# Performance work log

Hardware: AMD Instinct MI355X
Metric: run time of the kernel (lower is better)

## Reference

```python
import jax, jax.numpy as jnp
import numpy as np

ALPHA = 1.0
TOL = 1e-5
MAX_ITER = 50
M = 0.05  # monotonicity margin of MONSingleFc


def setup_inputs() -> dict:
    key = jax.random.key(0)
    kx, ku, kub, ka, kb = jax.random.split(key, 5)
    batch, in_dim, d = 65536, 128, 128
    x = jax.random.normal(kx, (batch, in_dim), jnp.float32)
    Uw = jax.random.normal(ku, (d, in_dim), jnp.float32) / np.sqrt(in_dim)
    ub = jax.random.normal(kub, (d,), jnp.float32) * 0.1
    A = jax.random.normal(ka, (d, d), jnp.float32) / np.sqrt(d)
    B = jax.random.normal(kb, (d, d), jnp.float32) / np.sqrt(d)
    return {"x": x, "Uw": Uw, "ub": ub, "A": A, "B": B}


def _multiply(z, A, B):
    # W z with W = (1-m) I - A^T A + B - B^T ; torch Linear applies z @ W^T
    return (1.0 - M) * z - (z @ A.T) @ A + z @ B.T - z @ B


def _solve_pr(bias, Winv):
    # Peaceman-Rachford fixed point: z = relu(W z + bias)
    def cond(s):
        _, _, err, it = s
        return (err > TOL) & (it < MAX_ITER)

    def body(s):
        z, u, _, it = s
        u12 = 2.0 * z - u
        z12 = (u12 + ALPHA * bias) @ Winv.T  # linear inverse solve
        u_new = 2.0 * z12 - u12
        zn = jax.nn.relu(u_new)
        err = jnp.linalg.norm(zn - z) / (1e-6 + jnp.linalg.norm(zn))
        return zn, u_new, err, it + 1

    z0 = jnp.zeros_like(bias)
    z, _, _, _ = jax.lax.while_loop(
        cond, body, (z0, z0, jnp.asarray(1.0, bias.dtype), 0)
    )
    return z


def reference(x, Uw, ub, A, B):
    d = A.shape[0]
    I = jnp.eye(d, dtype=A.dtype)
    W = (1.0 - M) * I - A.T @ A + B - B.T
    # init_inverse(1 + alpha, -alpha)
    Winv = jnp.linalg.inv((1.0 + ALPHA) * I - ALPHA * W)
    bias = x @ Uw.T + ub  # U(x)
    z_star = _solve_pr(bias, Winv)  # no-grad fixed point
    # final application: nonlin(linear(x, z*))
    return jax.nn.relu(bias + _multiply(z_star, A, B))
```

## Files before the change

### kernel.cpp

```cpp
#include <hip/hip_runtime.h>

#define D 128

typedef __attribute__((ext_vector_type(2))) float f32x2;
typedef __attribute__((ext_vector_type(4))) float f32x4;
typedef __attribute__((ext_vector_type(16))) float f32x16;
typedef __attribute__((ext_vector_type(2))) __fp16 fp16v2;
typedef __attribute__((ext_vector_type(4))) unsigned int u32x4;

__device__ __forceinline__ void split2(float a, float b, unsigned &hi, unsigned &lo) {
  fp16v2 h = __builtin_amdgcn_cvt_pkrtz(a, b);
  float ra = a - (float)h[0];
  float rb = b - (float)h[1];
  fp16v2 lv = __builtin_amdgcn_cvt_pkrtz(ra, rb);
  hi = __builtin_bit_cast(unsigned, h);
  lo = __builtin_bit_cast(unsigned, lv);
}

__device__ __forceinline__ void mma_acc(f32x16 &c, u32x4 a, u32x4 b) {
  asm volatile("s_nop 1\n\tv_mfma_f32_32x32x16_f16 %0, %1, %2, %0"
               : "+a"(c) : "v"(a), "v"(b));
}
__device__ __forceinline__ void mma_init(f32x16 &d, u32x4 a, u32x4 b,
                                         const f32x16 &cin) {
  asm volatile("s_nop 1\n\tv_mfma_f32_32x32x16_f16 %0, %1, %2, %3"
               : "=&a"(d) : "v"(a), "v"(b), "a"(cin));
}
__device__ __forceinline__ void mfma_fence() {
  asm volatile("s_nop 7\n\ts_nop 7\n\ts_nop 7");
}

__device__ __forceinline__ f32x16 zero16() {
  f32x16 z;
#pragma unroll
  for (int e = 0; e < 16; ++e) z[e] = 0.f;
  return z;
}

__global__ void wmat_kernel(const float* __restrict__ A, const float* __restrict__ B,
                            float* __restrict__ W, float* __restrict__ Mm) {
  const int i = blockIdx.x;
  const int j = threadIdx.x;
  float s = 0.f;
#pragma unroll 8
  for (int k = 0; k < D; ++k) s = fmaf(A[k * D + i], A[k * D + j], s);
  const float diag = (i == j) ? 1.f : 0.f;
  const float w = 0.95f * diag - s + B[i * D + j] - B[j * D + i];
  W[i * D + j] = w;
  Mm[i * D + j] = 2.f * diag - w;
}

__global__ __launch_bounds__(1024) void inv_kernel(const float* __restrict__ Mm,
                                                   float* __restrict__ Winv) {
  __shared__ float PROW[2][4][256];
  __shared__ __align__(16) float PC[2][D][4];
  const int t = threadIdx.x;
  const int c = t & 255;
  const int rb = t >> 8;
  const int r0 = rb * 32;
  float aug[32];
#pragma unroll
  for (int rr = 0; rr < 32; ++rr) {
    const int r = r0 + rr;
    aug[rr] = (c < D) ? Mm[r * D + c] : ((c - D == r) ? 1.f : 0.f);
  }
  if (rb == 0) {
#pragma unroll
    for (int s = 0; s < 4; ++s) PROW[0][s][c] = aug[s];
  }
  if (c < 4) {
#pragma unroll
    for (int rr = 0; rr < 32; ++rr) PC[0][r0 + rr][c] = aug[rr];
  }
  __syncthreads();
#pragma unroll
  for (int p = 0; p < 32; ++p) {
    const int buf = p & 1;
    const int kp = 4 * p;
    float p4[4], Bk[4][4], Bi[4][4];
#pragma unroll
    for (int s = 0; s < 4; ++s) p4[s] = PROW[buf][s][c];
#pragma unroll
    for (int s = 0; s < 4; ++s)
#pragma unroll
      for (int j = 0; j < 4; ++j) {
        Bk[s][j] = PROW[buf][s][kp + j];
        Bi[s][j] = (s == j) ? 1.f : 0.f;
      }
#pragma unroll
    for (int k = 0; k < 4; ++k) {
      const float ip = 1.f / Bk[k][k];
#pragma unroll
      for (int j = 0; j < 4; ++j) { Bk[k][j] *= ip; Bi[k][j] *= ip; }
#pragma unroll
      for (int s = 0; s < 4; ++s)
        if (s != k) {
          const float f = Bk[s][k];
#pragma unroll
          for (int j = 0; j < 4; ++j) {
            Bk[s][j] = fmaf(-f, Bk[k][j], Bk[s][j]);
            Bi[s][j] = fmaf(-f, Bi[k][j], Bi[s][j]);
          }
        }
    }
    float y[4];
#pragma unroll
    for (int s = 0; s < 4; ++s)
      y[s] = fmaf(Bi[s][0], p4[0], fmaf(Bi[s][1], p4[1],
             fmaf(Bi[s][2], p4[2], Bi[s][3] * p4[3])));
#pragma unroll
    for (int rr = 0; rr < 32; ++rr) {
      f32x4 c4 = *(const f32x4*)&PC[buf][r0 + rr][0];
      aug[rr] = fmaf(-c4[0], y[0], fmaf(-c4[1], y[1],
                fmaf(-c4[2], y[2], fmaf(-c4[3], y[3], aug[rr]))));
    }
    if (rb == (kp >> 5)) {
      const int base = kp & 31;
#pragma unroll
      for (int s = 0; s < 4; ++s) aug[base + s] = y[s];
    }
    if (p + 1 < 32) {
      const int kn = kp + 4;
      const int nb = buf ^ 1;
      if (rb == (kn >> 5)) {
        const int nbase = kn & 31;
#pragma unroll
        for (int s = 0; s < 4; ++s) PROW[nb][s][c] = aug[nbase + s];
      }
      if (c >= kn && c < kn + 4) {
#pragma unroll
        for (int rr = 0; rr < 32; ++rr) PC[nb][r0 + rr][c - kn] = aug[rr];
      }
    }
    __syncthreads();
  }
  if (c >= D) {
#pragma unroll
    for (int rr = 0; rr < 32; ++rr) Winv[(r0 + rr) * D + (c - D)] = aug[rr];
  }
}

__global__ __launch_bounds__(256, 1) void mon_main(
    const float* __restrict__ x, const float* __restrict__ Uw,
    const float* __restrict__ ub, const float* __restrict__ Wg,
    const float* __restrict__ Winvg, float* __restrict__ out) {

  __shared__ u32x4 AH[2048];
  __shared__ u32x4 AL[2048];

  const int tid = threadIdx.x;
  const int w = tid >> 6;
  const int l = tid & 63;
  const int l5 = l & 31;
  const int hi5 = l >> 5;
  const int rg0 = blockIdx.x * 256 + w * 64 + l5;
  const int rg1 = rg0 + 32;

  const int base_g = l5 * 16 + (hi5 ^ (l5 & 7));
  const float* xr0 = x + (size_t)rg0 * D + hi5 * 8;
  const float* xr1 = x + (size_t)rg1 * D + hi5 * 8;

  f32x16 acc[2][4];
  f32x16 bwC[2][4];
  float t[2][4][16];

  auto stageAB = [&](const float* __restrict__ M, float s) {
#pragma unroll
    for (int it = 0; it < 8; ++it) {
      const int G = tid + it * 256;
      const int i = G >> 4, g = G & 15;
      const float* src = M + i * D + g * 8;
      f32x4 a = *(const f32x4*)src;
      f32x4 b = *(const f32x4*)(src + 4);
      unsigned h0, l0_, h1, l1_, h2_, l2_, h3, l3_;
      split2(s * a[0], s * a[1], h0, l0_);
      split2(s * a[2], s * a[3], h1, l1_);
      split2(s * b[0], s * b[1], h2_, l2_);
      split2(s * b[2], s * b[3], h3, l3_);
      const int pg = g ^ (i & 7);
      AH[i * 16 + pg] = (u32x4){h0, h1, h2_, h3};
      AL[i * 16 + pg] = (u32x4){l0_, l1_, l2_, l3_};
    }
  };

  auto issue_kt = [&](const u32x4 (&ah)[4], const u32x4 (&al)[4],
                      const u32x4 (&fH)[2], const u32x4 (&fL)[2],
                      bool first, bool useC) {
    if (first) {
#pragma unroll
      for (int ft = 0; ft < 4; ++ft)
#pragma unroll
        for (int c = 0; c < 2; ++c) {
          if (useC) {
            mma_init(acc[c][ft], ah[ft], fH[c], bwC[c][ft]);
          } else {
            acc[c][ft] = zero16();
            mma_acc(acc[c][ft], ah[ft], fH[c]);
          }
        }
    } else {
#pragma unroll
      for (int ft = 0; ft < 4; ++ft)
#pragma unroll
        for (int c = 0; c < 2; ++c) mma_acc(acc[c][ft], ah[ft], fH[c]);
    }
#pragma unroll
    for (int ft = 0; ft < 4; ++ft)
#pragma unroll
      for (int c = 0; c < 2; ++c) mma_acc(acc[c][ft], ah[ft], fL[c]);
#pragma unroll
    for (int ft = 0; ft < 4; ++ft)
#pragma unroll
      for (int c = 0; c < 2; ++c) mma_acc(acc[c][ft], al[ft], fH[c]);
  };

  auto mfma_pass = [&](bool useAbs, bool useC) {
#pragma unroll
    for (int kt = 0; kt < 8; ++kt) {
      const int jt = kt >> 1;
      const int eb = 8 * (kt & 1);
      u32x4 fH[2], fL[2];
#pragma unroll
      for (int c = 0; c < 2; ++c) {
        unsigned oh[4], ol[4];
#pragma unroll
        for (int q = 0; q < 4; ++q) {
          float a0 = t[c][jt][eb + 2 * q], a1 = t[c][jt][eb + 2 * q + 1];
          if (useAbs) { a0 = __builtin_fabsf(a0); a1 = __builtin_fabsf(a1); }
          split2(a0, a1, oh[q], ol[q]);
        }
#pragma unroll
        for (int b = 0; b < 2; ++b) {
          auto rh = __builtin_amdgcn_permlane32_swap(oh[b], oh[2 + b], false, false);
          auto rl = __builtin_amdgcn_permlane32_swap(ol[b], ol[2 + b], false, false);
          fH[c][b] = rh[0]; fH[c][2 + b] = rh[1];
          fL[c][b] = rl[0]; fL[c][2 + b] = rl[1];
        }
      }
      const int gx = base_g ^ (2 * kt);
      u32x4 ah[4], al[4];
#pragma unroll
      for (int ft = 0; ft < 4; ++ft) {
        ah[ft] = AH[ft * 512 + gx];
        al[ft] = AL[ft * 512 + gx];
      }
      issue_kt(ah, al, fH, fL, kt == 0, useC);
    }
    mfma_fence();
  };

  auto x_pass = [&](bool useC) {
#pragma unroll
    for (int kt = 0; kt < 8; ++kt) {
      u32x4 fh[2], fl[2];
#pragma unroll
      for (int c = 0; c < 2; ++c) {
        const float* xrc = c ? xr1 : xr0;
        f32x4 xa = *(const f32x4*)(xrc + kt * 16);
        f32x4 xb = *(const f32x4*)(xrc + kt * 16 + 4);
        unsigned h0, l0_, h1, l1_, h2_, l2_, h3, l3_;
        split2(xa[0], xa[1], h0, l0_);
        split2(xa[2], xa[3], h1, l1_);
        split2(xb[0], xb[1], h2_, l2_);
        split2(xb[2], xb[3], h3, l3_);
        fh[c] = (u32x4){h0, h1, h2_, h3};
        fl[c] = (u32x4){l0_, l1_, l2_, l3_};
      }
      const int gx = base_g ^ (2 * kt);
      u32x4 ah[4], al[4];
#pragma unroll
      for (int ft = 0; ft < 4; ++ft) {
        ah[ft] = AH[ft * 512 + gx];
        al[ft] = AL[ft * 512 + gx];
      }
      issue_kt(ah, al, fh, fl, kt == 0, useC);
    }
    mfma_fence();
  };

  stageAB(Uw, 1.f);
  __syncthreads();
  x_pass(false);
#pragma unroll
  for (int c = 0; c < 2; ++c)
#pragma unroll
    for (int ft = 0; ft < 4; ++ft)
#pragma unroll
      for (int e2 = 0; e2 < 8; ++e2) {
        const int i0 = 32 * ft + 2 * (e2 & 1) + 8 * (e2 >> 1);
        f32x2 ubp = *(const f32x2*)(ub + i0 + 4 * hi5);
        t[c][ft][2 * e2] = acc[c][ft][2 * e2] + ubp[0];
        t[c][ft][2 * e2 + 1] = acc[c][ft][2 * e2 + 1] + ubp[1];
      }
  __syncthreads();
  stageAB(Winvg, 2.f);
  __syncthreads();

  mfma_pass(false, false);
#pragma unroll
  for (int c = 0; c < 2; ++c)
#pragma unroll
    for (int ft = 0; ft < 4; ++ft) {
      bwC[c][ft] = acc[c][ft];
#pragma unroll
      for (int e = 0; e < 16; ++e) t[c][ft][e] = acc[c][ft][e];
    }

#pragma unroll 1
  for (int it = 0; it < 48; ++it) {
    mfma_pass(true, true);
#pragma unroll
    for (int c = 0; c < 2; ++c)
#pragma unroll
      for (int ft = 0; ft < 4; ++ft)
#pragma unroll
        for (int e = 0; e < 16; ++e)
          t[c][ft][e] = acc[c][ft][e] - __builtin_fabsf(t[c][ft][e]);
  }

  mfma_pass(true, true);
#pragma unroll
  for (int c = 0; c < 2; ++c)
#pragma unroll
    for (int ft = 0; ft < 4; ++ft)
#pragma unroll
      for (int e = 0; e < 16; ++e)
        t[c][ft][e] = fmaxf(acc[c][ft][e] - __builtin_fabsf(t[c][ft][e]), 0.f);

  __syncthreads();
  stageAB(Wg, 1.f);
  __syncthreads();
  mfma_pass(false, false);
#pragma unroll
  for (int c = 0; c < 2; ++c)
#pragma unroll
    for (int ft = 0; ft < 4; ++ft) bwC[c][ft] = acc[c][ft];

  __syncthreads();
  stageAB(Uw, 1.f);
  __syncthreads();
  x_pass(true);
  float* op0 = out + (size_t)rg0 * D;
  float* op1 = out + (size_t)rg1 * D;
#pragma unroll
  for (int c = 0; c < 2; ++c) {
    float* op = c ? op1 : op0;
#pragma unroll
    for (int ft = 0; ft < 4; ++ft)
#pragma unroll
      for (int e2 = 0; e2 < 8; ++e2) {
        const int i0 = 32 * ft + 2 * (e2 & 1) + 8 * (e2 >> 1);
        f32x2 ubp = *(const f32x2*)(ub + i0 + 4 * hi5);
        float o0 = fmaxf(acc[c][ft][2 * e2] + ubp[0], 0.f);
        float o1 = fmaxf(acc[c][ft][2 * e2 + 1] + ubp[1], 0.f);
        *(f32x2*)(op + i0 + 4 * hi5) = (f32x2){o0, o1};
      }
  }
}

extern "C" void kernel_launch(void* const* d_in, const int* in_sizes, int n_in,
                              void* d_out, int out_size, void* d_ws, size_t ws_size,
                              hipStream_t stream) {
  const float* x = (const float*)d_in[0];
  const float* Uw = (const float*)d_in[1];
  const float* ub = (const float*)d_in[2];
  const float* A = (const float*)d_in[3];
  const float* B = (const float*)d_in[4];
  float* out = (float*)d_out;

  float* W = (float*)d_ws;
  float* Mm = W + D * D;
  float* Winv = W + 2 * D * D;

  wmat_kernel<<<D, D, 0, stream>>>(A, B, W, Mm);
  inv_kernel<<<1, 1024, 0, stream>>>(Mm, Winv);

  const int batch = in_sizes[0] / D;
  mon_main<<<batch / 256, 256, 0, stream>>>(x, Uw, ub, W, Winv, out);
}
```

Before: 430.8 us.

## Software-pipeline LDS A-fragment loads and fragment splitting across MFMA k-steps

Restructures the MFMA pass into a double-buffered pipeline: it prefetches the next k-step's A/AL fragments from shared memory and builds the next B fragments (fp16 hi/lo split plus permlane swaps) while the current k-step's MFMAs are issued. The goal is to hide LDS latency and the VALU fragment-building work behind matrix instructions in the 50-iteration solve loop. This costs extra VGPRs for the second buffer, which could push up register pressure or cause spills. Because the asm volatile MFMAs keep their order, the compiler's scheduling freedom is limited.

New measurement: 403.4 us. 6.4% less time.

```diff
diff --git a/kernel.cpp b/kernel.cpp
--- a/kernel.cpp
+++ b/kernel.cpp
@@ -163,6 +163,9 @@
   f32x16 acc[2][4];
   f32x16 bwC[2][4];
   float t[2][4][16];
+
+  u32x4 ahA[4], alA[4], ahB[4], alB[4];
+  u32x4 fHA[2], fLA[2], fHB[2], fLB[2];
 
   auto stageAB = [&](const float* __restrict__ M, float s) {
 #pragma unroll
@@ -183,68 +186,76 @@
     }
   };
 
-  auto issue_kt = [&](const u32x4 (&ah)[4], const u32x4 (&al)[4],
-                      const u32x4 (&fH)[2], const u32x4 (&fL)[2],
-                      bool first, bool useC) {
-    if (first) {
-#pragma unroll
-      for (int ft = 0; ft < 4; ++ft)
-#pragma unroll
-        for (int c = 0; c < 2; ++c) {
+  auto load_A = [&](int kt, u32x4 (&ah)[4], u32x4 (&al)[4]) {
+    const int gx = base_g ^ (2 * (kt & 7));
+#pragma unroll
+    for (int ft = 0; ft < 4; ++ft) {
+      ah[ft] = AH[ft * 512 + gx];
+      al[ft] = AL[ft * 512 + gx];
+    }
+  };
+
+  auto build_frags = [&](int kt, bool useAbs, u32x4 (&fH)[2], u32x4 (&fL)[2]) {
+    const int jt = kt >> 1;
+    const int eb = 8 * (kt & 1);
+#pragma unroll
+    for (int c = 0; c < 2; ++c) {
+      unsigned oh[4], ol[4];
+#pragma unroll
+      for (int q = 0; q < 4; ++q) {
+        float a0 = t[c][jt][eb + 2 * q], a1 = t[c][jt][eb + 2 * q + 1];
+        if (useAbs) { a0 = __builtin_fabsf(a0); a1 = __builtin_fabsf(a1); }
+        split2(a0, a1, oh[q], ol[q]);
+      }
+#pragma unroll
+      for (int b = 0; b < 2; ++b) {
+        auto rh = __builtin_amdgcn_permlane32_swap(oh[b], oh[2 + b], false, false);
+        auto rl = __builtin_amdgcn_permlane32_swap(ol[b], ol[2 + b], false, false);
+        fH[c][b] = rh[0]; fH[c][2 + b] = rh[1];
+        fL[c][b] = rl[0]; fL[c][2 + b] = rl[1];
+      }
+    }
+  };
+
+  auto term_first = [&](bool init, bool useC, u32x4 (&ah)[4], u32x4 (&fH)[2]) {
+#pragma unroll
+    for (int ft = 0; ft < 4; ++ft)
+#pragma unroll
+      for (int c = 0; c < 2; ++c) {
+        if (init) {
           if (useC) {
             mma_init(acc[c][ft], ah[ft], fH[c], bwC[c][ft]);
           } else {
             acc[c][ft] = zero16();
             mma_acc(acc[c][ft], ah[ft], fH[c]);
           }
+        } else {
+          mma_acc(acc[c][ft], ah[ft], fH[c]);
         }
-    } else {
-#pragma unroll
-      for (int ft = 0; ft < 4; ++ft)
-#pragma unroll
-        for (int c = 0; c < 2; ++c) mma_acc(acc[c][ft], ah[ft], fH[c]);
-    }
-#pragma unroll
-    for (int ft = 0; ft < 4; ++ft)
-#pragma unroll
-      for (int c = 0; c < 2; ++c) mma_acc(acc[c][ft], ah[ft], fL[c]);
-#pragma unroll
-    for (int ft = 0; ft < 4; ++ft)
-#pragma unroll
-      for (int c = 0; c < 2; ++c) mma_acc(acc[c][ft], al[ft], fH[c]);
+      }
+  };
+  auto term_mid = [&](u32x4 (&am)[4], u32x4 (&f)[2]) {
+#pragma unroll
+    for (int ft = 0; ft < 4; ++ft)
+#pragma unroll
+      for (int c = 0; c < 2; ++c) mma_acc(acc[c][ft], am[ft], f[c]);
   };
 
   auto mfma_pass = [&](bool useAbs, bool useC) {
-#pragma unroll
-    for (int kt = 0; kt < 8; ++kt) {
-      const int jt = kt >> 1;
-      const int eb = 8 * (kt & 1);
-      u32x4 fH[2], fL[2];
-#pragma unroll
-      for (int c = 0; c < 2; ++c) {
-        unsigned oh[4], ol[4];
-#pragma unroll
-        for (int q = 0; q < 4; ++q) {
-          float a0 = t[c][jt][eb + 2 * q], a1 = t[c][jt][eb + 2 * q + 1];
-          if (useAbs) { a0 = __builtin_fabsf(a0); a1 = __builtin_fabsf(a1); }
-          split2(a0, a1, oh[q], ol[q]);
-        }
-#pragma unroll
-        for (int b = 0; b < 2; ++b) {
-          auto rh = __builtin_amdgcn_permlane32_swap(oh[b], oh[2 + b], false, false);
-          auto rl = __builtin_amdgcn_permlane32_swap(ol[b], ol[2 + b], false, false);
-          fH[c][b] = rh[0]; fH[c][2 + b] = rh[1];
-          fL[c][b] = rl[0]; fL[c][2 + b] = rl[1];
-        }
-      }
-      const int gx = base_g ^ (2 * kt);
-      u32x4 ah[4], al[4];
-#pragma unroll
-      for (int ft = 0; ft < 4; ++ft) {
-        ah[ft] = AH[ft * 512 + gx];
-        al[ft] = AL[ft * 512 + gx];
-      }
-      issue_kt(ah, al, fH, fL, kt == 0, useC);
+    build_frags(0, useAbs, fHA, fLA);
+#pragma unroll
+    for (int kp = 0; kp < 4; ++kp) {
+      const int k0 = 2 * kp, k1 = 2 * kp + 1;
+      load_A(k0 + 1, ahB, alB);
+      term_first(k0 == 0, useC, ahA, fHA);
+      build_frags(k1, useAbs, fHB, fLB);
+      term_mid(ahA, fLA);
+      term_mid(alA, fHA);
+      load_A((k1 + 1) & 7, ahA, alA);
+      term_first(false, useC, ahB, fHB);
+      if (k1 < 7) build_frags(k1 + 1, useAbs, fHA, fLA);
+      term_mid(ahB, fLB);
+      term_mid(alB, fHB);
     }
     mfma_fence();
   };
@@ -266,14 +277,10 @@
         fh[c] = (u32x4){h0, h1, h2_, h3};
         fl[c] = (u32x4){l0_, l1_, l2_, l3_};
       }
-      const int gx = base_g ^ (2 * kt);
-      u32x4 ah[4], al[4];
-#pragma unroll
-      for (int ft = 0; ft < 4; ++ft) {
-        ah[ft] = AH[ft * 512 + gx];
-        al[ft] = AL[ft * 512 + gx];
-      }
-      issue_kt(ah, al, fh, fl, kt == 0, useC);
+      load_A(kt, ahA, alA);
+      term_first(kt == 0, useC, ahA, fh);
+      term_mid(ahA, fl);
+      term_mid(alA, fh);
     }
     mfma_fence();
   };
@@ -296,6 +303,7 @@
   stageAB(Winvg, 2.f);
   __syncthreads();
 
+  load_A(0, ahA, alA);
   mfma_pass(false, false);
 #pragma unroll
   for (int c = 0; c < 2; ++c)
@@ -330,6 +338,7 @@
   __syncthreads();
   stageAB(Wg, 1.f);
   __syncthreads();
+  load_A(0, ahA, alA);
   mfma_pass(false, false);
 #pragma unroll
   for (int c = 0; c < 2; ++c)
```
